# Performance work log

Hardware: AMD Instinct MI355X
Metric: run time of the kernel (lower is better)

Reference implementation:

```python
import jax, jax.numpy as jnp
import numpy as np

GROUPS = 32
EPS = 1e-6

def group_norm(x, gamma, beta):
    # x: [B,C,H,W]
    B, C, H, W = x.shape
    xg = x.reshape(B, GROUPS, C // GROUPS, H, W)
    mu = xg.mean(axis=(2, 3, 4), keepdims=True)
    var = xg.var(axis=(2, 3, 4), keepdims=True)
    xn = ((xg - mu) * jax.lax.rsqrt(var + EPS)).reshape(B, C, H, W)
    return xn * gamma[None, :, None, None] + beta[None, :, None, None]

def setup_inputs() -> dict:
    key = jax.random.key(0)
    ks = jax.random.split(key, 12)
    B, C, H, W = 4, 256, 64, 64
    s = 1.0 / np.sqrt(C)
    return {
        "x": jax.random.normal(ks[0], (B, C, H, W), jnp.float32),
        "gn_gamma": jnp.ones((C,), jnp.float32),
        "gn_beta": jnp.zeros((C,), jnp.float32),
        "wq": jax.random.normal(ks[1], (C, C), jnp.float32) * s,
        "bq": jnp.zeros((C,), jnp.float32),
        "wk": jax.random.normal(ks[2], (C, C), jnp.float32) * s,
        "bk": jnp.zeros((C,), jnp.float32),
        "wv": jax.random.normal(ks[3], (C, C), jnp.float32) * s,
        "bv": jnp.zeros((C,), jnp.float32),
        "wu": jax.random.normal(ks[4], (1, C), jnp.float32) * s,
        "bu": jnp.zeros((1,), jnp.float32),
        "wp": jax.random.normal(ks[5], (C, C), jnp.float32) * s,
        "bp": jnp.zeros((C,), jnp.float32),
    }

def reference(x, gn_gamma, gn_beta, wq, bq, wk, bk, wv, bv, wu, bu, wp, bp):
    B, C, H, W = x.shape
    hw = H * W
    hn = group_norm(x, gn_gamma, gn_beta)          # norm(x); context=x so same norm
    t = hn.reshape(B, C, hw).transpose(0, 2, 1)    # [B, hw, C]
    q = t @ wq.T + bq                              # 1x1 conv == per-token linear
    k = t @ wk.T + bk
    v = t @ wv.T + bv
    u_map = jax.nn.sigmoid(t @ wu.T + bu)          # [B, hw, 1]
    scale = jnp.asarray(C, x.dtype) ** -0.5
    scores = jnp.einsum('bic,bjc->bij', q, k) * scale * u_map.transpose(0, 2, 1)
    attn = jax.nn.softmax(scores, axis=2)          # softmax over keys j
    out = jnp.einsum('bij,bjc->bic', attn, v)      # [B, hw, C]
    out = (out @ wp.T + bp).transpose(0, 2, 1).reshape(B, C, H, W)
    return (x + out, u_map)
```

## Files before the change

kernel.cpp:

```cpp
#include <hip/hip_runtime.h>
#include <cstdint>

#define B_ 4
#define C_ 256
#define HW_ 4096
#define CPG_ 8
#define M_TOT 16384
#define SCALE 0.0625f
#define LOG2E 1.44269504088896f
#define FLASH_LDS 133120

typedef __attribute__((ext_vector_type(4))) float f32x4;
typedef __attribute__((ext_vector_type(16))) float f32x16;
typedef __attribute__((ext_vector_type(8))) unsigned short u16x8;
typedef __attribute__((ext_vector_type(4))) unsigned short u16x4;
typedef __attribute__((ext_vector_type(4))) unsigned int u32x4;
typedef __attribute__((ext_vector_type(8))) __bf16 bf16x8;

static __device__ __forceinline__ unsigned short f2bf(float f) {
  unsigned int u = __builtin_bit_cast(unsigned int, f);
  u += 0x7fffu + ((u >> 16) & 1u);
  return (unsigned short)(u >> 16);
}
static __device__ __forceinline__ float bf2f(unsigned short s) {
  return __builtin_bit_cast(float, ((unsigned int)s) << 16);
}
static __device__ __forceinline__ bf16x8 ldbf8(const unsigned short* p) {
  return __builtin_bit_cast(bf16x8, *(const u16x8*)p);
}
static __device__ __forceinline__ bf16x8 cvt8(const float* p) {
  f32x4 a = *(const f32x4*)p;
  f32x4 b = *(const f32x4*)(p + 4);
  u16x8 r;
  r[0] = f2bf(a[0]); r[1] = f2bf(a[1]); r[2] = f2bf(a[2]); r[3] = f2bf(a[3]);
  r[4] = f2bf(b[0]); r[5] = f2bf(b[1]); r[6] = f2bf(b[2]); r[7] = f2bf(b[3]);
  return __builtin_bit_cast(bf16x8, r);
}
static __device__ __forceinline__ void gload16(const void* g, void* l) {
  __builtin_amdgcn_global_load_lds(
      (const __attribute__((address_space(1))) unsigned int*)g,
      (__attribute__((address_space(3))) unsigned int*)l, 16, 0, 0);
}
static __device__ __forceinline__ unsigned cvtpk(float lo, float hi) {
  unsigned r;
  asm("v_cvt_pk_bf16_f32 %0, %1, %2" : "=v"(r) : "v"(lo), "v"(hi));
  return r;
}

__global__ __launch_bounds__(256) void gn_kernel(const float* __restrict__ x,
    const float* __restrict__ gamma, const float* __restrict__ beta,
    unsigned short* __restrict__ t) {
  int bg = blockIdx.x;
  int b = bg >> 5, g = bg & 31;
  const float* xp = x + ((size_t)(b * C_ + g * CPG_)) * HW_;
  float s = 0.f, ss = 0.f;
  for (int i = threadIdx.x; i < CPG_ * HW_; i += 256) {
    float v = xp[i]; s += v; ss += v * v;
  }
#pragma unroll
  for (int m = 32; m; m >>= 1) { s += __shfl_xor(s, m); ss += __shfl_xor(ss, m); }
  __shared__ float red[8];
  if ((threadIdx.x & 63) == 0) { red[threadIdx.x >> 6] = s; red[4 + (threadIdx.x >> 6)] = ss; }
  __syncthreads();
  float S = red[0] + red[1] + red[2] + red[3];
  float SS = red[4] + red[5] + red[6] + red[7];
  float mean = S * (1.f / 32768.f);
  float var = SS * (1.f / 32768.f) - mean * mean;
  float rs = rsqrtf(var + 1e-6f);
  float gam[CPG_], bet[CPG_];
#pragma unroll
  for (int cc = 0; cc < CPG_; ++cc) {
    float gm = gamma[g * CPG_ + cc];
    gam[cc] = gm * rs;
    bet[cc] = beta[g * CPG_ + cc] - mean * gm * rs;
  }
  for (int sp = threadIdx.x; sp < HW_; sp += 256) {
    u16x8 o;
#pragma unroll
    for (int cc = 0; cc < CPG_; ++cc) {
      float v = xp[cc * HW_ + sp];
      o[cc] = f2bf(v * gam[cc] + bet[cc]);
    }
    *(u16x8*)(t + ((size_t)(b * HW_ + sp)) * C_ + g * CPG_) = o;
  }
}

__global__ __launch_bounds__(256) void u_kernel(const unsigned short* __restrict__ t,
    const float* __restrict__ wu, const float* __restrict__ bu,
    float* __restrict__ uout) {
  int w = threadIdx.x >> 6, l = threadIdx.x & 63;
  int tok = blockIdx.x * 4 + w;
  u16x4 tv = *(const u16x4*)(t + (size_t)tok * C_ + l * 4);
  f32x4 wv4 = *(const f32x4*)(wu + l * 4);
  float d = bf2f(tv[0]) * wv4[0] + bf2f(tv[1]) * wv4[1] +
            bf2f(tv[2]) * wv4[2] + bf2f(tv[3]) * wv4[3];
#pragma unroll
  for (int m = 32; m; m >>= 1) d += __shfl_xor(d, m);
  if (l == 0) uout[tok] = 1.f / (1.f + __expf(-(d + bu[0])));
}

__global__ __launch_bounds__(256, 2) void qkv_kernel(const unsigned short* __restrict__ t,
    const float* __restrict__ wq, const float* __restrict__ wk, const float* __restrict__ wv,
    const float* __restrict__ bq, const float* __restrict__ bk, const float* __restrict__ bv,
    const float* __restrict__ uu,
    unsigned short* __restrict__ q, unsigned short* __restrict__ k,
    unsigned short* __restrict__ vt) {
  int mblk = blockIdx.x, nblk = blockIdx.y;
  int wsel = nblk >> 2;
  int n0 = (nblk & 3) * 64;
  const float* W = wsel == 0 ? wq : (wsel == 1 ? wk : wv);
  const float* bias = wsel == 0 ? bq : (wsel == 1 ? bk : bv);
  __shared__ unsigned short WL[64][264];
  int tid = threadIdx.x;
#pragma unroll
  for (int p = 0; p < 8; ++p) {
    int row = p * 8 + (tid >> 5);
    int kc0 = (tid & 31) * 8;
    *(bf16x8*)&WL[row][kc0] = cvt8(W + (size_t)(n0 + row) * C_ + kc0);
  }
  __syncthreads();
  int wid = tid >> 6, l = tid & 63;
  int lr = l & 15, lg = l >> 4;
  int row = mblk * 64 + wid * 16 + lr;
  f32x4 acc[4] = {};
  const unsigned short* ap = t + (size_t)row * C_ + lg * 8;
#pragma unroll
  for (int kc = 0; kc < 8; ++kc) {
    bf16x8 a = ldbf8(ap + kc * 32);
#pragma unroll
    for (int j = 0; j < 4; ++j) {
      bf16x8 bb = ldbf8(&WL[j * 16 + lr][kc * 32 + lg * 8]);
      acc[j] = __builtin_amdgcn_mfma_f32_16x16x32_bf16(a, bb, acc[j], 0, 0, 0);
    }
  }
  if (wsel < 2) {
    unsigned short* dst = wsel ? k : q;
    float su[4] = {1.f, 1.f, 1.f, 1.f};
    if (wsel == 1) {
      f32x4 u4 = *(const f32x4*)(uu + mblk * 64 + wid * 16 + lg * 4);
      su[0] = SCALE * LOG2E * u4[0]; su[1] = SCALE * LOG2E * u4[1];
      su[2] = SCALE * LOG2E * u4[2]; su[3] = SCALE * LOG2E * u4[3];
    }
#pragma unroll
    for (int j = 0; j < 4; ++j) {
      int col = n0 + j * 16 + lr;
      float bv_ = bias[col];
#pragma unroll
      for (int r = 0; r < 4; ++r)
        dst[(size_t)(mblk * 64 + wid * 16 + lg * 4 + r) * C_ + col] =
            f2bf((acc[j][r] + bv_) * su[r]);
    }
  } else {
    __shared__ float lds[64][65];
#pragma unroll
    for (int j = 0; j < 4; ++j) {
      float bv_ = bias[n0 + j * 16 + lr];
#pragma unroll
      for (int r = 0; r < 4; ++r)
        lds[wid * 16 + lg * 4 + r][j * 16 + lr] = acc[j][r] + bv_;
    }
    __syncthreads();
    int bb_ = (mblk * 64) >> 12;
    int s0 = (mblk * 64) & 4095;
    int ss = tid & 63, cc0 = tid >> 6;
    for (int cc = cc0; cc < 64; cc += 4)
      vt[((size_t)(bb_ * C_ + n0 + cc)) * HW_ + s0 + ss] = f2bf(lds[ss][cc]);
  }
}

__global__ __launch_bounds__(512, 2) void flash_kernel(const unsigned short* __restrict__ q,
    const unsigned short* __restrict__ k, const unsigned short* __restrict__ vt,
    unsigned short* __restrict__ o) {
  extern __shared__ char smem[];
  float* cmb_m = (float*)(smem + 131072);
  float* cmb_l = (float*)(smem + 131584);
  float* facw  = (float*)(smem + 132096);
  float* scrL  = (float*)(smem + 132608);

  int blk = blockIdx.x;
  int b = blk >> 6;
  int qrow0 = (blk & 63) * 64;
  int tid = threadIdx.x;
  int wid = tid >> 6, l = tid & 63;
  int l5 = l & 31, hi = l >> 5;

  const unsigned short* kb = k + (size_t)b * HW_ * C_;
  const unsigned short* vb = vt + (size_t)b * C_ * HW_;

  float mrow = -1e30f, lrow = 0.f;
  f32x16 oa[8];

  if (wid >= 4) {
    int role = wid - 4;
    int sh = role & 1;
    bool isK = role < 2;
    int w_ = l >> 2;
    int w0_ = w_ & 1, w1_ = (w_ >> 1) & 1, w2_ = (w_ >> 2) & 1, w3_ = (w_ >> 3) & 1;
    int koffb = (l & 3) * 8;
#define STG(IT, BUFN)                                                           \
    {                                                                           \
      int key0n = sh * 2048 + (IT) * 32;                                        \
      if (isK) {                                                                \
        _Pragma("unroll")                                                       \
        for (int j = 0; j < 16; ++j) {                                          \
          int key = j * 2 + hi;                                                 \
          const unsigned short* g =                                             \
              kb + (size_t)(key0n + key) * C_ + ((l5 * 8) ^ (key * 8));         \
          gload16(g, smem + (BUFN) * 32768 + sh * 16384 + j * 1024);            \
        }                                                                       \
      } else {                                                                  \
        _Pragma("unroll")                                                       \
        for (int j = 0; j < 16; ++j) {                                          \
          int j0 = j & 1;                                                       \
          int ch = (j << 4) | (w3_ << 3) | ((w2_ ^ j0) << 2) |                  \
                   ((w1_ ^ w3_) << 1) | (w0_ ^ w2_ ^ j0);                       \
          int ke = koffb ^ ((ch & 3) << 3);                                     \
          const unsigned short* g = vb + (size_t)ch * HW_ + key0n + ke;         \
          gload16(g, smem + 65536 + (BUFN) * 32768 + sh * 16384 + j * 1024);    \
        }                                                                       \
      }                                                                         \
    }
    STG(0, 0);
    __syncthreads();
    for (int it = 0; it < 64; ++it) {
      if (it + 1 < 64) STG(it + 1, (it + 1) & 1);
      __syncthreads();
    }
#undef STG
  } else {
    int h = wid >> 1, qs = wid & 1;
    bf16x8 qreg[16];
    {
      const unsigned short* qp =
          q + ((size_t)b * HW_ + qrow0 + qs * 32 + l5) * C_ + hi * 8;
#pragma unroll
      for (int cc = 0; cc < 16; ++cc) qreg[cc] = ldbf8(qp + cc * 16);
    }
#pragma unroll
    for (int ct = 0; ct < 8; ++ct)
#pragma unroll
      for (int r = 0; r < 16; ++r) oa[ct][r] = 0.f;
    __syncthreads();

    int kx = l5 << 4;
    int vbase = (l5 * 64) ^ ((l5 >> 2) << 6);
    int ko0 = (hi * 16) ^ ((l & 3) << 4);
    int ko1 = (32 + hi * 16) ^ ((l & 3) << 4);

    for (int it = 0; it < 64; ++it) {
      int buf = it & 1;
      const char* KB = smem + buf * 32768 + h * 16384;
      f32x16 s;
#pragma unroll
      for (int r = 0; r < 16; ++r) s[r] = 0.f;
#pragma unroll
      for (int cc = 0; cc < 16; ++cc) {
        bf16x8 kf = ldbf8((const unsigned short*)(KB + l5 * 512 +
                                                  ((cc * 32 + hi * 16) ^ kx)));
        s = __builtin_amdgcn_mfma_f32_32x32x16_bf16(kf, qreg[cc], s, 0, 0, 0);
      }
      float mxl = s[0];
#pragma unroll
      for (int r = 1; r < 16; ++r) mxl = fmaxf(mxl, s[r]);
      float mx = fmaxf(mxl, __shfl_xor(mxl, 32));
      if (!__all(mx <= mrow + 11.f)) {
        float mnew = fmaxf(mrow, mx);
        float scr = exp2f(mrow - mnew);
        mrow = mnew;
        lrow *= scr;
        if (hi == 0) scrL[wid * 32 + l5] = scr;
        float sr[16];
#pragma unroll
        for (int r = 0; r < 16; ++r)
          sr[r] = scrL[wid * 32 + (r & 3) + 8 * (r >> 2) + 4 * hi];
#pragma unroll
        for (int ct = 0; ct < 8; ++ct)
#pragma unroll
          for (int r = 0; r < 16; ++r) oa[ct][r] *= sr[r];
      }
      unsigned wp[8];
#pragma unroll
      for (int rp = 0; rp < 8; ++rp) {
        float e0 = exp2f(s[2 * rp] - mrow);
        float e1 = exp2f(s[2 * rp + 1] - mrow);
        lrow += e0 + e1;
        wp[rp] = cvtpk(e0, e1);
      }
      unsigned sx[8];
#pragma unroll
      for (int rp = 0; rp < 8; ++rp) sx[rp] = (unsigned)__shfl_xor((int)wp[rp], 32);
      bool hib = (hi != 0);
      u32x4 pa0u = {hib ? sx[2] : wp[0], hib ? sx[3] : wp[1],
                    hib ? wp[2] : sx[0], hib ? wp[3] : sx[1]};
      u32x4 pa1u = {hib ? sx[6] : wp[4], hib ? sx[7] : wp[5],
                    hib ? wp[6] : sx[4], hib ? wp[7] : sx[5]};
      bf16x8 pa0 = __builtin_bit_cast(bf16x8, pa0u);
      bf16x8 pa1 = __builtin_bit_cast(bf16x8, pa1u);
      const char* VB = smem + 65536 + buf * 32768 + h * 16384;
#pragma unroll
      for (int ct = 0; ct < 8; ++ct) {
        bf16x8 v0 = ldbf8((const unsigned short*)(VB + ct * 2048 + vbase + ko0));
        bf16x8 v1 = ldbf8((const unsigned short*)(VB + ct * 2048 + vbase + ko1));
        oa[ct] = __builtin_amdgcn_mfma_f32_32x32x16_bf16(pa0, v0, oa[ct], 0, 0, 0);
        oa[ct] = __builtin_amdgcn_mfma_f32_32x32x16_bf16(pa1, v1, oa[ct], 0, 0, 0);
      }
      __syncthreads();
    }
  }

  float l_all = 0.f;
  if (wid < 4) {
    l_all = lrow + __shfl_xor(lrow, 32);
    if (hi == 0) { cmb_m[wid * 32 + l5] = mrow; cmb_l[wid * 32 + l5] = l_all; }
  }
  __syncthreads();
  if (wid < 4) {
    float mo = cmb_m[(wid ^ 2) * 32 + l5];
    float lo = cmb_l[(wid ^ 2) * 32 + l5];
    float M = fmaxf(mrow, mo);
    float el = exp2f(mrow - M), eo = exp2f(mo - M);
    float fac = el / (l_all * el + lo * eo);
    if (hi == 0) facw[wid * 32 + l5] = fac;
    float fr[16];
#pragma unroll
    for (int r = 0; r < 16; ++r)
      fr[r] = facw[wid * 32 + (r & 3) + 8 * (r >> 2) + 4 * hi];
    float* Ow = (float*)(smem + wid * 32768);
#pragma unroll
    for (int ct = 0; ct < 8; ++ct)
#pragma unroll
      for (int r = 0; r < 16; ++r) {
        int qr = (r & 3) + 8 * (r >> 2) + 4 * hi;
        Ow[qr * 256 + ct * 32 + l5] = oa[ct][r] * fr[r];
      }
  }
  __syncthreads();
  for (int e = tid; e < 2048; e += 512) {
    int row = e >> 5;
    int c8 = (e & 31) * 8;
    int qs_ = row >> 5, q_ = row & 31;
    const float* p0 = (const float*)(smem + qs_ * 32768) + q_ * 256 + c8;
    const float* p1 = (const float*)(smem + (2 + qs_) * 32768) + q_ * 256 + c8;
    u16x8 ov;
#pragma unroll
    for (int j = 0; j < 8; ++j) ov[j] = f2bf(p0[j] + p1[j]);
    *(u16x8*)(o + ((size_t)b * HW_ + qrow0 + row) * C_ + c8) = ov;
  }
}

__global__ __launch_bounds__(256, 2) void proj_kernel(const unsigned short* __restrict__ o,
    const float* __restrict__ wp, const float* __restrict__ bp,
    const float* __restrict__ x, float* __restrict__ y) {
  int mblk = blockIdx.x, nblk = blockIdx.y;
  int n0 = nblk * 64;
  __shared__ unsigned short WL[64][264];
  int tid = threadIdx.x;
#pragma unroll
  for (int p = 0; p < 8; ++p) {
    int row = p * 8 + (tid >> 5);
    int kc0 = (tid & 31) * 8;
    *(bf16x8*)&WL[row][kc0] = cvt8(wp + (size_t)(n0 + row) * C_ + kc0);
  }
  __syncthreads();
  int wid = tid >> 6, l = tid & 63;
  int lr = l & 15, lg = l >> 4;
  int row = mblk * 64 + wid * 16 + lr;
  f32x4 acc[4] = {};
  const unsigned short* ap = o + (size_t)row * C_ + lg * 8;
#pragma unroll
  for (int kc = 0; kc < 8; ++kc) {
    bf16x8 a = ldbf8(ap + kc * 32);
#pragma unroll
    for (int j = 0; j < 4; ++j) {
      bf16x8 bb = ldbf8(&WL[j * 16 + lr][kc * 32 + lg * 8]);
      acc[j] = __builtin_amdgcn_mfma_f32_16x16x32_bf16(a, bb, acc[j], 0, 0, 0);
    }
  }
  __shared__ float lds[64][65];
#pragma unroll
  for (int j = 0; j < 4; ++j) {
    float bv_ = bp[n0 + j * 16 + lr];
#pragma unroll
    for (int r = 0; r < 4; ++r)
      lds[wid * 16 + lg * 4 + r][j * 16 + lr] = acc[j][r] + bv_;
  }
  __syncthreads();
  int bb_ = (mblk * 64) >> 12;
  int s0 = (mblk * 64) & 4095;
  int ss = tid & 63, cc0 = tid >> 6;
  for (int cc = cc0; cc < 64; cc += 4) {
    size_t idx = ((size_t)(bb_ * C_ + n0 + cc)) * HW_ + s0 + ss;
    y[idx] = x[idx] + lds[ss][cc];
  }
}

extern "C" void kernel_launch(void* const* d_in, const int* in_sizes, int n_in,
                              void* d_out, int out_size, void* d_ws, size_t ws_size,
                              hipStream_t stream) {
  const float* x     = (const float*)d_in[0];
  const float* gamma = (const float*)d_in[1];
  const float* beta  = (const float*)d_in[2];
  const float* wq    = (const float*)d_in[3];
  const float* bq    = (const float*)d_in[4];
  const float* wk    = (const float*)d_in[5];
  const float* bk    = (const float*)d_in[6];
  const float* wv    = (const float*)d_in[7];
  const float* bv    = (const float*)d_in[8];
  const float* wu    = (const float*)d_in[9];
  const float* bu    = (const float*)d_in[10];
  const float* wp    = (const float*)d_in[11];
  const float* bp    = (const float*)d_in[12];

  float* y = (float*)d_out;
  float* uout = y + (size_t)B_ * C_ * HW_;

  unsigned short* t  = (unsigned short*)d_ws;
  unsigned short* qb = t + (size_t)M_TOT * C_;
  unsigned short* kk = qb + (size_t)M_TOT * C_;
  unsigned short* vt = kk + (size_t)M_TOT * C_;

  hipFuncSetAttribute((const void*)flash_kernel,
                      hipFuncAttributeMaxDynamicSharedMemorySize, FLASH_LDS);

  gn_kernel<<<128, 256, 0, stream>>>(x, gamma, beta, t);
  u_kernel<<<4096, 256, 0, stream>>>(t, wu, bu, uout);
  qkv_kernel<<<dim3(256, 12), 256, 0, stream>>>(t, wq, wk, wv, bq, bk, bv, uout, qb, kk, vt);
  flash_kernel<<<256, 512, FLASH_LDS, stream>>>(qb, kk, vt, t);
  proj_kernel<<<dim3(256, 4), 256, 0, stream>>>(t, wp, bp, x, y);
}
```

Before: 194.3 us.

## Reuse activation tiles across Q/K/V, remap flash blocks per XCD, split MFMA chains

The QKV kernel now loads each token tile's activations once into registers and loops over the three weight matrices. This cuts the grid from 12 to 4 column blocks and avoids reading the activations three times. The flash kernel remaps block indices so each XCD handles a single batch's K/V, which is meant to improve L2 locality. Its score accumulation is split into two independent MFMA chains to shorten the dependency chain. In exchange, the QKV kernel has fewer blocks and serial work per block, with extra barriers.

```diff
diff --git a/kernel.cpp b/kernel.cpp
--- a/kernel.cpp
+++ b/kernel.cpp
@@ -106,65 +106,70 @@
     unsigned short* __restrict__ q, unsigned short* __restrict__ k,
     unsigned short* __restrict__ vt) {
   int mblk = blockIdx.x, nblk = blockIdx.y;
-  int wsel = nblk >> 2;
-  int n0 = (nblk & 3) * 64;
-  const float* W = wsel == 0 ? wq : (wsel == 1 ? wk : wv);
-  const float* bias = wsel == 0 ? bq : (wsel == 1 ? bk : bv);
+  int n0 = nblk * 64;
   __shared__ unsigned short WL[64][264];
+  __shared__ float lds[64][65];
   int tid = threadIdx.x;
-#pragma unroll
-  for (int p = 0; p < 8; ++p) {
-    int row = p * 8 + (tid >> 5);
-    int kc0 = (tid & 31) * 8;
-    *(bf16x8*)&WL[row][kc0] = cvt8(W + (size_t)(n0 + row) * C_ + kc0);
-  }
-  __syncthreads();
   int wid = tid >> 6, l = tid & 63;
   int lr = l & 15, lg = l >> 4;
   int row = mblk * 64 + wid * 16 + lr;
-  f32x4 acc[4] = {};
+  bf16x8 af[8];
   const unsigned short* ap = t + (size_t)row * C_ + lg * 8;
 #pragma unroll
-  for (int kc = 0; kc < 8; ++kc) {
-    bf16x8 a = ldbf8(ap + kc * 32);
-#pragma unroll
-    for (int j = 0; j < 4; ++j) {
-      bf16x8 bb = ldbf8(&WL[j * 16 + lr][kc * 32 + lg * 8]);
-      acc[j] = __builtin_amdgcn_mfma_f32_16x16x32_bf16(a, bb, acc[j], 0, 0, 0);
-    }
-  }
-  if (wsel < 2) {
-    unsigned short* dst = wsel ? k : q;
-    float su[4] = {1.f, 1.f, 1.f, 1.f};
-    if (wsel == 1) {
-      f32x4 u4 = *(const f32x4*)(uu + mblk * 64 + wid * 16 + lg * 4);
-      su[0] = SCALE * LOG2E * u4[0]; su[1] = SCALE * LOG2E * u4[1];
-      su[2] = SCALE * LOG2E * u4[2]; su[3] = SCALE * LOG2E * u4[3];
-    }
-#pragma unroll
-    for (int j = 0; j < 4; ++j) {
-      int col = n0 + j * 16 + lr;
-      float bv_ = bias[col];
-#pragma unroll
-      for (int r = 0; r < 4; ++r)
-        dst[(size_t)(mblk * 64 + wid * 16 + lg * 4 + r) * C_ + col] =
-            f2bf((acc[j][r] + bv_) * su[r]);
-    }
-  } else {
-    __shared__ float lds[64][65];
-#pragma unroll
-    for (int j = 0; j < 4; ++j) {
-      float bv_ = bias[n0 + j * 16 + lr];
-#pragma unroll
-      for (int r = 0; r < 4; ++r)
-        lds[wid * 16 + lg * 4 + r][j * 16 + lr] = acc[j][r] + bv_;
+  for (int kc = 0; kc < 8; ++kc) af[kc] = ldbf8(ap + kc * 32);
+  f32x4 u4 = *(const f32x4*)(uu + mblk * 64 + wid * 16 + lg * 4);
+
+#pragma unroll 1
+  for (int w = 0; w < 3; ++w) {
+    const float* W = w == 0 ? wq : (w == 1 ? wk : wv);
+    const float* bias = w == 0 ? bq : (w == 1 ? bk : bv);
+    if (w) __syncthreads();
+#pragma unroll
+    for (int p = 0; p < 8; ++p) {
+      int rw = p * 8 + (tid >> 5);
+      int kc0 = (tid & 31) * 8;
+      *(bf16x8*)&WL[rw][kc0] = cvt8(W + (size_t)(n0 + rw) * C_ + kc0);
     }
     __syncthreads();
-    int bb_ = (mblk * 64) >> 12;
-    int s0 = (mblk * 64) & 4095;
-    int ss = tid & 63, cc0 = tid >> 6;
-    for (int cc = cc0; cc < 64; cc += 4)
-      vt[((size_t)(bb_ * C_ + n0 + cc)) * HW_ + s0 + ss] = f2bf(lds[ss][cc]);
+    f32x4 acc[4] = {};
+#pragma unroll
+    for (int kc = 0; kc < 8; ++kc)
+#pragma unroll
+      for (int j = 0; j < 4; ++j) {
+        bf16x8 bb = ldbf8(&WL[j * 16 + lr][kc * 32 + lg * 8]);
+        acc[j] = __builtin_amdgcn_mfma_f32_16x16x32_bf16(af[kc], bb, acc[j], 0, 0, 0);
+      }
+    if (w < 2) {
+      unsigned short* dst = w ? k : q;
+      float su[4] = {1.f, 1.f, 1.f, 1.f};
+      if (w == 1) {
+        su[0] = SCALE * LOG2E * u4[0]; su[1] = SCALE * LOG2E * u4[1];
+        su[2] = SCALE * LOG2E * u4[2]; su[3] = SCALE * LOG2E * u4[3];
+      }
+#pragma unroll
+      for (int j = 0; j < 4; ++j) {
+        int col = n0 + j * 16 + lr;
+        float bv_ = bias[col];
+#pragma unroll
+        for (int r = 0; r < 4; ++r)
+          dst[(size_t)(mblk * 64 + wid * 16 + lg * 4 + r) * C_ + col] =
+              f2bf((acc[j][r] + bv_) * su[r]);
+      }
+    } else {
+#pragma unroll
+      for (int j = 0; j < 4; ++j) {
+        float bv_ = bias[n0 + j * 16 + lr];
+#pragma unroll
+        for (int r = 0; r < 4; ++r)
+          lds[wid * 16 + lg * 4 + r][j * 16 + lr] = acc[j][r] + bv_;
+      }
+      __syncthreads();
+      int bb_ = (mblk * 64) >> 12;
+      int s0 = (mblk * 64) & 4095;
+      int ss = tid & 63, cc0 = tid >> 6;
+      for (int cc = cc0; cc < 64; cc += 4)
+        vt[((size_t)(bb_ * C_ + n0 + cc)) * HW_ + s0 + ss] = f2bf(lds[ss][cc]);
+    }
   }
 }
 
@@ -178,8 +183,9 @@
   float* scrL  = (float*)(smem + 132608);
 
   int blk = blockIdx.x;
-  int b = blk >> 6;
-  int qrow0 = (blk & 63) * 64;
+  int xcd = blk & 7, slot = blk >> 3;
+  int b = xcd >> 1;
+  int qrow0 = (((xcd & 1) << 5) | slot) * 64;
   int tid = threadIdx.x;
   int wid = tid >> 6, l = tid & 63;
   int l5 = l & 31, hi = l >> 5;
@@ -250,15 +256,19 @@
     for (int it = 0; it < 64; ++it) {
       int buf = it & 1;
       const char* KB = smem + buf * 32768 + h * 16384;
-      f32x16 s;
-#pragma unroll
-      for (int r = 0; r < 16; ++r) s[r] = 0.f;
-#pragma unroll
-      for (int cc = 0; cc < 16; ++cc) {
-        bf16x8 kf = ldbf8((const unsigned short*)(KB + l5 * 512 +
-                                                  ((cc * 32 + hi * 16) ^ kx)));
-        s = __builtin_amdgcn_mfma_f32_32x32x16_bf16(kf, qreg[cc], s, 0, 0, 0);
-      }
+      f32x16 sa, sb;
+#pragma unroll
+      for (int r = 0; r < 16; ++r) { sa[r] = 0.f; sb[r] = 0.f; }
+#pragma unroll
+      for (int cc = 0; cc < 16; cc += 2) {
+        bf16x8 kf0 = ldbf8((const unsigned short*)(KB + l5 * 512 +
+                                                   ((cc * 32 + hi * 16) ^ kx)));
+        bf16x8 kf1 = ldbf8((const unsigned short*)(KB + l5 * 512 +
+                                                   (((cc + 1) * 32 + hi * 16) ^ kx)));
+        sa = __builtin_amdgcn_mfma_f32_32x32x16_bf16(kf0, qreg[cc], sa, 0, 0, 0);
+        sb = __builtin_amdgcn_mfma_f32_32x32x16_bf16(kf1, qreg[cc + 1], sb, 0, 0, 0);
+      }
+      f32x16 s = sa + sb;
       float mxl = s[0];
 #pragma unroll
       for (int r = 1; r < 16; ++r) mxl = fmaxf(mxl, s[r]);
@@ -424,7 +434,7 @@
 
   gn_kernel<<<128, 256, 0, stream>>>(x, gamma, beta, t);
   u_kernel<<<4096, 256, 0, stream>>>(t, wu, bu, uout);
-  qkv_kernel<<<dim3(256, 12), 256, 0, stream>>>(t, wq, wk, wv, bq, bk, bv, uout, qb, kk, vt);
+  qkv_kernel<<<dim3(256, 4), 256, 0, stream>>>(t, wq, wk, wv, bq, bk, bv, uout, qb, kk, vt);
   flash_kernel<<<256, 512, FLASH_LDS, stream>>>(qb, kk, vt, t);
   proj_kernel<<<dim3(256, 4), 256, 0, stream>>>(t, wp, bp, x, y);
 }
```

New measurement: 197.1 us. No clear change (+1.4%).
